# Performance work log

Hardware: AMD Instinct MI355X
Metric: run time of the kernel (lower is better)

The kernel has to match this reference:

```python
import jax, jax.numpy as jnp
import numpy as np

N_SRC, N_TGT, N_EDGES = 100000, 50000, 600000
IN_CH, OUT_CH = 128, 128
NUM_EDGE_TYPES, NUM_NODE_TYPES = 7, 4


def setup_inputs() -> dict:
    key = jax.random.key(0)
    ks = jax.random.split(key, 9)
    x_src = jax.random.normal(ks[0], (N_SRC, IN_CH), dtype=jnp.float32)
    x_target = jax.random.normal(ks[1], (N_TGT, IN_CH), dtype=jnp.float32)
    # PyG Linear: y = x @ W.T (+ b); W has shape (out, in)
    rel_w = jax.random.normal(ks[2], (NUM_EDGE_TYPES, OUT_CH, IN_CH), dtype=jnp.float32) * 0.05
    root_w = jax.random.normal(ks[3], (NUM_NODE_TYPES, OUT_CH, IN_CH), dtype=jnp.float32) * 0.05
    root_b = jax.random.normal(ks[4], (NUM_NODE_TYPES, OUT_CH), dtype=jnp.float32) * 0.05
    edge_src = jax.random.randint(ks[5], (N_EDGES,), 0, N_SRC, dtype=jnp.int32)
    edge_dst = jax.random.randint(ks[6], (N_EDGES,), 0, N_TGT, dtype=jnp.int32)
    edge_type = jax.random.randint(ks[7], (N_EDGES,), 0, NUM_EDGE_TYPES, dtype=jnp.int32)
    target_node_type = jax.random.randint(ks[8], (N_TGT,), 0, NUM_NODE_TYPES, dtype=jnp.int32)
    return {
        "x_src": x_src, "x_target": x_target,
        "rel_w": rel_w, "root_w": root_w, "root_b": root_b,
        "edge_src": edge_src, "edge_dst": edge_dst,
        "edge_type": edge_type, "target_node_type": target_node_type,
    }


def reference(x_src, x_target, rel_w, root_w, root_b,
              edge_src, edge_dst, edge_type, target_node_type):
    n_tgt = x_target.shape[0]
    num_rel = rel_w.shape[0]
    num_ntypes = root_w.shape[0]
    # Gather source features once for all edges: (E, in)
    msg = x_src[edge_src]
    out = jnp.zeros((n_tgt, rel_w.shape[1]), dtype=x_target.dtype)
    # Per-relation linear transform + scatter-MEAN over that relation's edges
    # (matches one propagate(aggr='mean') call per edge type: nodes with no
    #  incoming edges of type r contribute 0 for that relation).
    for r in range(num_rel):
        mask = (edge_type == r).astype(msg.dtype)  # (E,)
        y = (msg * mask[:, None]) @ rel_w[r].T     # (E, out)
        s = jax.ops.segment_sum(y, edge_dst, num_segments=n_tgt)
        cnt = jax.ops.segment_sum(mask, edge_dst, num_segments=n_tgt)
        out = out + s / jnp.maximum(cnt, 1.0)[:, None]
    # Per-node-type root linear (with bias), masked add
    for t in range(num_ntypes):
        m = (target_node_type == t)
        root = x_target @ root_w[t].T + root_b[t]
        out = out + jnp.where(m[:, None], root, 0.0)
    return out
```

## Files before the change

### kernel.cpp

```cpp
#include <hip/hip_runtime.h>

#define NSRC 100000
#define NTGT 50000
#define NE   600000
#define CH   128
#define NREL 7
#define NTYP 4
#define NP   (NREL * NTGT)
#define NB   ((NP + 1023) / 1024)
#define AGGB (NP / 16)
#define GEMB 1563

typedef __attribute__((ext_vector_type(4))) float f32x4;
typedef __attribute__((ext_vector_type(8))) short bf16x8;
typedef unsigned int uint;
typedef unsigned short ushort;

static constexpr long long NXB4 = (long long)NSRC * CH / 4;
static constexpr long long NXT4 = (long long)NTGT * CH / 4;
static constexpr long long NWR4 = (long long)NREL * CH * CH / 4;
static constexpr long long NWT4 = (long long)NTYP * CH * CH / 4;
static constexpr int CONVB  = (int)((NXB4 + NXT4 + NWR4 + NWT4 + 255) / 256);
static constexpr int COUNTB = (NE + 255) / 256;

static constexpr size_t A256(size_t x) { return (x + 255) & ~(size_t)255; }
static constexpr size_t CNT_O   = 0;
static constexpr size_t BSE_O   = A256(CNT_O + (size_t)NP * 4);
static constexpr size_t EOFF_O  = A256(BSE_O + (size_t)NB * 4);
static constexpr size_t CUR_O   = A256(EOFF_O + (size_t)(NP + 1) * 4);
static constexpr size_t SEDGE_O = A256(CUR_O + (size_t)NP * 4);
static constexpr size_t WB_O    = A256(SEDGE_O + (size_t)NE * 4);
static constexpr size_t XB_O    = A256(WB_O + (size_t)(NREL + NTYP) * CH * CH * 2);
static constexpr size_t XTB_O   = A256(XB_O + (size_t)NSRC * CH * 2);
static constexpr size_t MEAN_O  = A256(XTB_O + (size_t)NTGT * CH * 2);

#define GLOAD_LDS(gp, lp) __builtin_amdgcn_global_load_lds( \
    (const __attribute__((address_space(1))) void*)(gp), \
    (__attribute__((address_space(3))) void*)(lp), 16, 0, 0)
#define WAITVM0()   asm volatile("s_waitcnt vmcnt(0)" ::: "memory")
#define WAITLGKM0() asm volatile("s_waitcnt lgkmcnt(0)" ::: "memory")
#define SB0()       __builtin_amdgcn_sched_barrier(0)

__device__ __forceinline__ uint bfpack(float a, float b) {
  uint ua = __float_as_uint(a); ua = (ua + 0x7fff + ((ua >> 16) & 1)) >> 16;
  uint ub = __float_as_uint(b); ub = (ub + 0x7fff + ((ub >> 16) & 1)) >> 16;
  return ua | (ub << 16);
}
__device__ __forceinline__ ushort f2b(float x) {
  uint u = __float_as_uint(x);
  return (ushort)((u + 0x7fff + ((u >> 16) & 1)) >> 16);
}
__device__ __forceinline__ float bl(uint u) { return __uint_as_float(u << 16); }
__device__ __forceinline__ float bh(uint u) { return __uint_as_float(u & 0xffff0000u); }

__global__ __launch_bounds__(256) void k_pre(
    const float* __restrict__ xsrc, const float* __restrict__ xt,
    const float* __restrict__ relw, const float* __restrict__ rootw,
    ushort* __restrict__ xb, ushort* __restrict__ xtb, ushort* __restrict__ wb,
    const int* __restrict__ edst, const int* __restrict__ etyp,
    int* __restrict__ cnt) {
  int bx = blockIdx.x;
  if (bx < CONVB) {
    long long i4 = (long long)bx * 256 + threadIdx.x;
    const float* src; ushort* dst; long long off;
    if (i4 < NXB4) { src = xsrc; dst = xb; off = i4; }
    else if (i4 < NXB4 + NXT4) { src = xt; dst = xtb; off = i4 - NXB4; }
    else if (i4 < NXB4 + NXT4 + NWR4) { src = relw; dst = wb; off = i4 - NXB4 - NXT4; }
    else if (i4 < NXB4 + NXT4 + NWR4 + NWT4) {
      src = rootw; dst = wb + (size_t)NREL * CH * CH; off = i4 - NXB4 - NXT4 - NWR4;
    } else return;
    float4 v = *(const float4*)(src + off * 4);
    uint lo = (uint)f2b(v.x) | ((uint)f2b(v.y) << 16);
    uint hi = (uint)f2b(v.z) | ((uint)f2b(v.w) << 16);
    uint2 o = make_uint2(lo, hi);
    *(uint2*)(dst + off * 4) = o;
    return;
  }
  bx -= CONVB;
  int i = bx * 256 + threadIdx.x;
  if (i < NE) atomicAdd(&cnt[etyp[i] * NTGT + edst[i]], 1);
}

__global__ __launch_bounds__(256) void k_s1(const int* __restrict__ cnt,
                                            int* __restrict__ bsE) {
  __shared__ int sE[256];
  int t = threadIdx.x, p0 = blockIdx.x * 1024 + t * 4;
  int e = 0;
#pragma unroll
  for (int j = 0; j < 4; ++j) {
    int p = p0 + j;
    if (p < NP) e += cnt[p];
  }
  sE[t] = e; __syncthreads();
  for (int s = 128; s > 0; s >>= 1) {
    if (t < s) sE[t] += sE[t + s];
    __syncthreads();
  }
  if (t == 0) bsE[blockIdx.x] = sE[0];
}

__global__ __launch_bounds__(512) void k_s23(const int* __restrict__ cnt,
                                             const int* __restrict__ bsE,
                                             int* __restrict__ eoff,
                                             int* __restrict__ cur) {
  __shared__ int sE[512];
  __shared__ int sBase;
  int t = threadIdx.x;
  int e = (t < NB) ? bsE[t] : 0;
  sE[t] = e; __syncthreads();
  for (int s = 1; s < 512; s <<= 1) {
    int a = 0; if (t >= s) a = sE[t - s];
    __syncthreads();
    sE[t] += a;
    __syncthreads();
  }
  if (t == blockIdx.x) sBase = sE[t] - e;
  __syncthreads();
  int base0 = sBase;
  int p0 = blockIdx.x * 1024 + t * 2;
  int c0 = (p0 < NP) ? cnt[p0] : 0;
  int c1 = (p0 + 1 < NP) ? cnt[p0 + 1] : 0;
  int e2 = c0 + c1;
  sE[t] = e2; __syncthreads();
  for (int s = 1; s < 512; s <<= 1) {
    int a = 0; if (t >= s) a = sE[t - s];
    __syncthreads();
    sE[t] += a;
    __syncthreads();
  }
  int baseE = base0 + sE[t] - e2;
  if (p0 < NP)     { eoff[p0] = baseE;          cur[p0] = baseE; }
  if (p0 + 1 < NP) { eoff[p0 + 1] = baseE + c0; cur[p0 + 1] = baseE + c0; }
  if (p0 + 1 == NP - 1) eoff[NP] = baseE + c0 + c1;
}

__global__ __launch_bounds__(256) void k_esort(
    const int* __restrict__ esrc, const int* __restrict__ edst,
    const int* __restrict__ etyp, int* __restrict__ cur,
    int* __restrict__ sedge) {
  int i = blockIdx.x * 256 + threadIdx.x;
  if (i < NE) {
    int p = etyp[i] * NTGT + edst[i];
    int pos = atomicAdd(&cur[p], 1);
    sedge[pos] = esrc[i];
  }
}

__global__ __launch_bounds__(256) void k_agg(
    const ushort* __restrict__ xb, const int* __restrict__ sedge,
    const int* __restrict__ eoff, ushort* __restrict__ mean) {
  int tid = threadIdx.x;
  int g = tid >> 4, l16 = tid & 15;
  int p = blockIdx.x * 16 + g;
  int lo = eoff[p], hi = eoff[p + 1];
  int cnt = hi - lo;
  float acc[8];
#pragma unroll
  for (int c = 0; c < 8; ++c) acc[c] = 0.f;
  int base = lo;
  while (base < hi) {
    int nb = hi - base; if (nb > 16) nb = 16;
    int sv = (l16 < nb) ? sedge[base + l16] : 0;
    for (int j = 0; j < nb; ++j) {
      int s = __shfl(sv, (g & 3) * 16 + j);
      uint4 v = *(const uint4*)(xb + (size_t)s * CH + (l16 << 3));
      acc[0] += bl(v.x); acc[1] += bh(v.x);
      acc[2] += bl(v.y); acc[3] += bh(v.y);
      acc[4] += bl(v.z); acc[5] += bh(v.z);
      acc[6] += bl(v.w); acc[7] += bh(v.w);
    }
    base += 16;
  }
  float inv = (cnt > 0) ? __builtin_amdgcn_rcpf((float)cnt) : 0.f;
  uint4 o;
  o.x = bfpack(acc[0] * inv, acc[1] * inv);
  o.y = bfpack(acc[2] * inv, acc[3] * inv);
  o.z = bfpack(acc[4] * inv, acc[5] * inv);
  o.w = bfpack(acc[6] * inv, acc[7] * inv);
  *(uint4*)(mean + (size_t)p * CH + (l16 << 3)) = o;
}

__global__ __launch_bounds__(256) void k_gemm(
    const ushort* __restrict__ mean, const ushort* __restrict__ xtb,
    const ushort* __restrict__ wb, const int* __restrict__ ntyp,
    const float* __restrict__ rootb, float* __restrict__ out) {
  __shared__ ushort As[4 * 2048];
  int wv = threadIdx.x >> 6, ln = threadIdx.x & 63;
  ushort* strip = As + wv * 2048;
  int m = ln & 15, quad = ln >> 4;
  int w = blockIdx.x * 4 + wv;
  int tile = w >> 1, half = w & 1;
  int dstbase = tile * 16;
  if (dstbase >= NTGT) return;
  int ct0 = half * 4;

  f32x4 acc[4];
#pragma unroll
  for (int ct = 0; ct < 4; ++ct) acc[ct] = (f32x4){0.f, 0.f, 0.f, 0.f};

  for (int ph = 0; ph < NREL; ++ph) {
    const ushort* gb = mean + ((size_t)ph * NTGT + dstbase) * CH;
    WAITLGKM0(); SB0();
#pragma unroll
    for (int t4 = 0; t4 < 4; ++t4) {
      int i = t4 * 4 + quad;
      const ushort* gp = gb + (size_t)i * CH + ((m ^ i) << 3);
      GLOAD_LDS(gp, strip + t4 * 512);
    }
    WAITVM0(); SB0();
    bf16x8 aF[4];
#pragma unroll
    for (int ks = 0; ks < 4; ++ks) {
      int c = ks * 4 + quad;
      aF[ks] = *(const bf16x8*)&strip[(m * 16 + (c ^ m)) << 3];
    }
    const ushort* W = wb + (size_t)ph * CH * CH;
#pragma unroll
    for (int ct = 0; ct < 4; ++ct) {
      int n = (ct0 + ct) * 16 + m;
#pragma unroll
      for (int ks = 0; ks < 4; ++ks) {
        bf16x8 bF = *(const bf16x8*)(W + (size_t)n * CH + ks * 32 + quad * 8);
        acc[ct] = __builtin_amdgcn_mfma_f32_16x16x32_bf16(aF[ks], bF, acc[ct], 0, 0, 0);
      }
    }
  }

  WAITLGKM0(); SB0();
#pragma unroll
  for (int t4 = 0; t4 < 4; ++t4) {
    int i = t4 * 4 + quad;
    const ushort* gp = xtb + (size_t)(dstbase + i) * CH + ((m ^ i) << 3);
    GLOAD_LDS(gp, strip + t4 * 512);
  }
  WAITVM0(); SB0();
  int myt = ntyp[dstbase + m];
  union { uint u[4]; bf16x8 v; } aT[4];
#pragma unroll
  for (int ks = 0; ks < 4; ++ks) {
    int c = ks * 4 + quad;
    aT[ks].v = *(const bf16x8*)&strip[(m * 16 + (c ^ m)) << 3];
  }
#pragma unroll
  for (int ty = 0; ty < NTYP; ++ty) {
    union { uint u[4]; bf16x8 v; } aM[4];
#pragma unroll
    for (int ks = 0; ks < 4; ++ks)
#pragma unroll
      for (int k2 = 0; k2 < 4; ++k2)
        aM[ks].u[k2] = (myt == ty) ? aT[ks].u[k2] : 0u;
    const ushort* W = wb + (size_t)(NREL + ty) * CH * CH;
#pragma unroll
    for (int ct = 0; ct < 4; ++ct) {
      int n = (ct0 + ct) * 16 + m;
#pragma unroll
      for (int ks = 0; ks < 4; ++ks) {
        bf16x8 bF = *(const bf16x8*)(W + (size_t)n * CH + ks * 32 + quad * 8);
        acc[ct] = __builtin_amdgcn_mfma_f32_16x16x32_bf16(aM[ks].v, bF, acc[ct], 0, 0, 0);
      }
    }
  }

#pragma unroll
  for (int reg = 0; reg < 4; ++reg) {
    int row = quad * 4 + reg;
    int dst = dstbase + row;
    int tt = ntyp[dst];
    const float* rb = rootb + (size_t)tt * CH;
#pragma unroll
    for (int ct = 0; ct < 4; ++ct) {
      int col = (ct0 + ct) * 16 + m;
      out[(size_t)dst * CH + col] = acc[ct][reg] + rb[col];
    }
  }
}

extern "C" void kernel_launch(void* const* d_in, const int* in_sizes, int n_in,
                              void* d_out, int out_size, void* d_ws, size_t ws_size,
                              hipStream_t stream) {
  (void)in_sizes; (void)n_in; (void)out_size; (void)ws_size;
  const float* xsrc  = (const float*)d_in[0];
  const float* xt    = (const float*)d_in[1];
  const float* relw  = (const float*)d_in[2];
  const float* rootw = (const float*)d_in[3];
  const float* rootb = (const float*)d_in[4];
  const int* esrc = (const int*)d_in[5];
  const int* edst = (const int*)d_in[6];
  const int* etyp = (const int*)d_in[7];
  const int* ntyp = (const int*)d_in[8];
  float* out = (float*)d_out;

  char* ws = (char*)d_ws;
  int*   cnt    = (int*)(ws + CNT_O);
  int*   bsE    = (int*)(ws + BSE_O);
  int*   eoff   = (int*)(ws + EOFF_O);
  int*   cur    = (int*)(ws + CUR_O);
  int*   sedge  = (int*)(ws + SEDGE_O);
  ushort* wb    = (ushort*)(ws + WB_O);
  ushort* xb    = (ushort*)(ws + XB_O);
  ushort* xtb   = (ushort*)(ws + XTB_O);
  ushort* mean  = (ushort*)(ws + MEAN_O);

  hipMemsetAsync(cnt, 0, (size_t)NP * 4, stream);
  k_pre<<<dim3(CONVB + COUNTB), dim3(256), 0, stream>>>(
      xsrc, xt, relw, rootw, xb, xtb, wb, edst, etyp, cnt);
  k_s1<<<dim3(NB), dim3(256), 0, stream>>>(cnt, bsE);
  k_s23<<<dim3(NB), dim3(512), 0, stream>>>(cnt, bsE, eoff, cur);
  k_esort<<<dim3(COUNTB), dim3(256), 0, stream>>>(esrc, edst, etyp, cur, sedge);
  k_agg<<<dim3(AGGB), dim3(256), 0, stream>>>(xb, sedge, eoff, mean);
  k_gemm<<<dim3(GEMB), dim3(256), 0, stream>>>(
      mean, xtb, wb, ntyp, rootb, out);
}
```

Baseline: 392.5 us.

## Load GEMM A fragments directly to registers with prefetch; unroll aggregation loop by eight

The GEMM kernel stops staging the A tile through LDS with global_load_lds and explicit waits. Each lane now loads its bf16x8 fragments straight from global memory, and the next relation's (or x_target's) fragments are prefetched while the current MFMAs run. The aggregation kernel processes edges in fixed chunks of eight with a fully unrolled inner loop and per-edge guards, so more gathers can be in flight. The trade-off is higher register pressure and uncoalesced direct fragment loads, plus wasted guarded iterations for low-degree nodes.

```diff
diff --git a/kernel.cpp b/kernel.cpp
--- a/kernel.cpp
+++ b/kernel.cpp
@@ -34,13 +34,6 @@
 static constexpr size_t XTB_O   = A256(XB_O + (size_t)NSRC * CH * 2);
 static constexpr size_t MEAN_O  = A256(XTB_O + (size_t)NTGT * CH * 2);
 
-#define GLOAD_LDS(gp, lp) __builtin_amdgcn_global_load_lds( \
-    (const __attribute__((address_space(1))) void*)(gp), \
-    (__attribute__((address_space(3))) void*)(lp), 16, 0, 0)
-#define WAITVM0()   asm volatile("s_waitcnt vmcnt(0)" ::: "memory")
-#define WAITLGKM0() asm volatile("s_waitcnt lgkmcnt(0)" ::: "memory")
-#define SB0()       __builtin_amdgcn_sched_barrier(0)
-
 __device__ __forceinline__ uint bfpack(float a, float b) {
   uint ua = __float_as_uint(a); ua = (ua + 0x7fff + ((ua >> 16) & 1)) >> 16;
   uint ub = __float_as_uint(b); ub = (ub + 0x7fff + ((ub >> 16) & 1)) >> 16;
@@ -52,6 +45,13 @@
 }
 __device__ __forceinline__ float bl(uint u) { return __uint_as_float(u << 16); }
 __device__ __forceinline__ float bh(uint u) { return __uint_as_float(u & 0xffff0000u); }
+
+__device__ __forceinline__ void add8(float* a, uint4 u) {
+  a[0] += bl(u.x); a[1] += bh(u.x);
+  a[2] += bl(u.y); a[3] += bh(u.y);
+  a[4] += bl(u.z); a[5] += bh(u.z);
+  a[6] += bl(u.w); a[7] += bh(u.w);
+}
 
 __global__ __launch_bounds__(256) void k_pre(
     const float* __restrict__ xsrc, const float* __restrict__ xt,
@@ -157,19 +157,16 @@
   float acc[8];
 #pragma unroll
   for (int c = 0; c < 8; ++c) acc[c] = 0.f;
-  int base = lo;
-  while (base < hi) {
-    int nb = hi - base; if (nb > 16) nb = 16;
-    int sv = (l16 < nb) ? sedge[base + l16] : 0;
-    for (int j = 0; j < nb; ++j) {
+  for (int base = lo; base < hi; base += 8) {
+    int sv = (l16 < 8 && base + l16 < hi) ? sedge[base + l16] : 0;
+#pragma unroll
+    for (int j = 0; j < 8; ++j) {
       int s = __shfl(sv, (g & 3) * 16 + j);
-      uint4 v = *(const uint4*)(xb + (size_t)s * CH + (l16 << 3));
-      acc[0] += bl(v.x); acc[1] += bh(v.x);
-      acc[2] += bl(v.y); acc[3] += bh(v.y);
-      acc[4] += bl(v.z); acc[5] += bh(v.z);
-      acc[6] += bl(v.w); acc[7] += bh(v.w);
-    }
-    base += 16;
+      if (base + j < hi) {
+        uint4 v = *(const uint4*)(xb + (size_t)s * CH + (l16 << 3));
+        add8(acc, v);
+      }
+    }
   }
   float inv = (cnt > 0) ? __builtin_amdgcn_rcpf((float)cnt) : 0.f;
   uint4 o;
@@ -184,9 +181,7 @@
     const ushort* __restrict__ mean, const ushort* __restrict__ xtb,
     const ushort* __restrict__ wb, const int* __restrict__ ntyp,
     const float* __restrict__ rootb, float* __restrict__ out) {
-  __shared__ ushort As[4 * 2048];
   int wv = threadIdx.x >> 6, ln = threadIdx.x & 63;
-  ushort* strip = As + wv * 2048;
   int m = ln & 15, quad = ln >> 4;
   int w = blockIdx.x * 4 + wv;
   int tile = w >> 1, half = w & 1;
@@ -198,21 +193,22 @@
 #pragma unroll
   for (int ct = 0; ct < 4; ++ct) acc[ct] = (f32x4){0.f, 0.f, 0.f, 0.f};
 
+  const ushort* a0 = mean + (size_t)(dstbase + m) * CH + (quad << 3);
+  const ushort* at = xtb + (size_t)(dstbase + m) * CH + (quad << 3);
+
+  bf16x8 aF[4], aN[4];
+#pragma unroll
+  for (int ks = 0; ks < 4; ++ks)
+    aF[ks] = *(const bf16x8*)(a0 + ks * 32);
+
+#pragma unroll
   for (int ph = 0; ph < NREL; ++ph) {
-    const ushort* gb = mean + ((size_t)ph * NTGT + dstbase) * CH;
-    WAITLGKM0(); SB0();
-#pragma unroll
-    for (int t4 = 0; t4 < 4; ++t4) {
-      int i = t4 * 4 + quad;
-      const ushort* gp = gb + (size_t)i * CH + ((m ^ i) << 3);
-      GLOAD_LDS(gp, strip + t4 * 512);
-    }
-    WAITVM0(); SB0();
-    bf16x8 aF[4];
 #pragma unroll
     for (int ks = 0; ks < 4; ++ks) {
-      int c = ks * 4 + quad;
-      aF[ks] = *(const bf16x8*)&strip[(m * 16 + (c ^ m)) << 3];
+      const ushort* an = (ph + 1 < NREL)
+          ? (a0 + (size_t)(ph + 1) * NTGT * CH + ks * 32)
+          : (at + ks * 32);
+      aN[ks] = *(const bf16x8*)an;
     }
     const ushort* W = wb + (size_t)ph * CH * CH;
 #pragma unroll
@@ -224,31 +220,21 @@
         acc[ct] = __builtin_amdgcn_mfma_f32_16x16x32_bf16(aF[ks], bF, acc[ct], 0, 0, 0);
       }
     }
-  }
-
-  WAITLGKM0(); SB0();
-#pragma unroll
-  for (int t4 = 0; t4 < 4; ++t4) {
-    int i = t4 * 4 + quad;
-    const ushort* gp = xtb + (size_t)(dstbase + i) * CH + ((m ^ i) << 3);
-    GLOAD_LDS(gp, strip + t4 * 512);
-  }
-  WAITVM0(); SB0();
+#pragma unroll
+    for (int ks = 0; ks < 4; ++ks) aF[ks] = aN[ks];
+  }
+
   int myt = ntyp[dstbase + m];
-  union { uint u[4]; bf16x8 v; } aT[4];
-#pragma unroll
-  for (int ks = 0; ks < 4; ++ks) {
-    int c = ks * 4 + quad;
-    aT[ks].v = *(const bf16x8*)&strip[(m * 16 + (c ^ m)) << 3];
-  }
 #pragma unroll
   for (int ty = 0; ty < NTYP; ++ty) {
     union { uint u[4]; bf16x8 v; } aM[4];
 #pragma unroll
-    for (int ks = 0; ks < 4; ++ks)
+    for (int ks = 0; ks < 4; ++ks) {
+      union { bf16x8 v; uint u[4]; } sU; sU.v = aF[ks];
 #pragma unroll
       for (int k2 = 0; k2 < 4; ++k2)
-        aM[ks].u[k2] = (myt == ty) ? aT[ks].u[k2] : 0u;
+        aM[ks].u[k2] = (myt == ty) ? sU.u[k2] : 0u;
+    }
     const ushort* W = wb + (size_t)(NREL + ty) * CH * CH;
 #pragma unroll
     for (int ct = 0; ct < 4; ++ct) {
```

Measured after the change: 391.2 us. Within noise of the previous version (-0.3%).
